# Performance work log

Measured on AMD Instinct MI355X. Metric: run time of the kernel, lower is better.

Reference implementation:

```python
import jax, jax.numpy as jnp
import numpy as np

DIM = 2560
HEADS = 64
HEAD_DIM = 40
TEMB = 512
FF = 4 * DIM
B = 1
S = 1248
TXT = 224
EPS = 1e-6


def _ln(x, eps=EPS):
    # LayerNorm over last dim, no affine (elementwise_affine=False)
    m = jnp.mean(x, axis=-1, keepdims=True)
    v = jnp.mean(jnp.square(x - m), axis=-1, keepdims=True)
    return (x - m) * jax.lax.rsqrt(v + eps)


def setup_inputs() -> dict:
    key = jax.random.key(0)
    ks = jax.random.split(key, 10)
    w = 0.02
    return {
        "hidden_states": jax.random.normal(ks[0], (B, S, DIM), jnp.float32),
        "emb": jax.random.normal(ks[1], (B, TEMB), jnp.float32),
        "attention_mask": jnp.zeros((B, 1, S, S), jnp.float32),
        "adaln_w": jax.random.normal(ks[2], (TEMB, 12 * DIM), jnp.float32) * w,
        "adaln_b": jnp.zeros((12 * DIM,), jnp.float32),
        "qkv_w": jax.random.normal(ks[3], (DIM, 3 * DIM), jnp.float32) * w,
        "qkv_b": jnp.zeros((3 * DIM,), jnp.float32),
        "out_w": jax.random.normal(ks[4], (DIM, DIM), jnp.float32) * w,
        "out_b": jnp.zeros((DIM,), jnp.float32),
        "ff1_w": jax.random.normal(ks[5], (DIM, FF), jnp.float32) * w,
        "ff1_b": jnp.zeros((FF,), jnp.float32),
        "ff2_w": jax.random.normal(ks[6], (FF, DIM), jnp.float32) * w,
        "ff2_b": jnp.zeros((DIM,), jnp.float32),
        "text_length": TXT,
    }


def reference(hidden_states, emb, attention_mask, adaln_w, adaln_b, qkv_w, qkv_b,
              out_w, out_b, ff1_w, ff1_b, ff2_w, ff2_b, text_length):
    b, s, d = hidden_states.shape
    t = text_length

    # adaLN: SiLU -> Linear(time_embed_dim, 12*dim), chunk into 12 [B, dim] pieces
    ada = jax.nn.silu(emb) @ adaln_w + adaln_b
    (sh_msa_i, sc_msa_i, g_msa_i, sh_mlp_i, sc_mlp_i, g_mlp_i,
     sh_msa_t, sc_msa_t, g_msa_t, sh_mlp_t, sc_mlp_t, g_mlp_t) = jnp.split(ada, 12, axis=1)

    def mod(x, shift, scale):
        return x * (1.0 + scale[:, None, :]) + shift[:, None, :]

    # --- attention block ---
    ai = _ln(hidden_states)
    ai = jnp.concatenate([mod(ai[:, :t], sh_msa_t, sc_msa_t),
                          mod(ai[:, t:], sh_msa_i, sc_msa_i)], axis=1)

    qkv = ai @ qkv_w + qkv_b                              # [B, S, 3*D]
    q, k, v = jnp.split(qkv, 3, axis=-1)
    q = q.reshape(b, s, HEADS, HEAD_DIM).transpose(0, 2, 1, 3)  # [B, H, S, hd]
    k = k.reshape(b, s, HEADS, HEAD_DIM).transpose(0, 2, 1, 3)
    v = v.reshape(b, s, HEADS, HEAD_DIM).transpose(0, 2, 1, 3)

    q = _ln(q)  # per-head QK layernorm
    k = _ln(k)

    scores = jnp.einsum("bhqd,bhkd->bhqk", q, k) / (HEAD_DIM ** 0.5)
    scores = scores + attention_mask
    probs = jax.nn.softmax(scores, axis=-1)
    ctx = jnp.einsum("bhqk,bhkd->bhqd", probs, v)
    ctx = ctx.transpose(0, 2, 1, 3).reshape(b, s, d)
    attn_out = ctx @ out_w + out_b

    h = jnp.concatenate([hidden_states[:, :t] + g_msa_t[:, None, :] * attn_out[:, :t],
                         hidden_states[:, t:] + g_msa_i[:, None, :] * attn_out[:, t:]], axis=1)

    # --- MLP block ---
    mi = _ln(h)
    mi = jnp.concatenate([mod(mi[:, :t], sh_mlp_t, sc_mlp_t),
                          mod(mi[:, t:], sh_mlp_i, sc_mlp_i)], axis=1)
    mo = jax.nn.gelu(mi @ ff1_w + ff1_b, approximate=True) @ ff2_w + ff2_b

    h = jnp.concatenate([h[:, :t] + g_mlp_t[:, None, :] * mo[:, :t],
                         h[:, t:] + g_mlp_i[:, None, :] * mo[:, t:]], axis=1)
    return h
```

## Files before the change

### kernel.cpp

```cpp
#include <hip/hip_runtime.h>
#include <cstdint>

typedef float f32x4 __attribute__((ext_vector_type(4)));
typedef __bf16 bf16x8 __attribute__((ext_vector_type(8)));
typedef __bf16 bf16x4 __attribute__((ext_vector_type(4)));

#define S_LEN 1248
#define S_PAD 1280
#define DIMD 2560
#define NHEAD 64
#define HDIM 40
#define T3 7680

__device__ __forceinline__ f32x4 mfma16(bf16x8 a, bf16x8 b, f32x4 c) {
  return __builtin_amdgcn_mfma_f32_16x16x32_bf16(a, b, c, 0, 0, 0);
}

__global__ void k_adaln(const float* __restrict__ emb, const float* __restrict__ W,
                        const float* __restrict__ b, float* __restrict__ ada) {
  __shared__ __attribute__((aligned(16))) float se[512];
  int tid = threadIdx.x;
  for (int i = tid; i < 512; i += 64) {
    float e = emb[i];
    se[i] = e / (1.f + __expf(-e));
  }
  __syncthreads();
  int col = blockIdx.x * 64 + tid;
  float acc = 0.f;
  #pragma unroll 8
  for (int k = 0; k < 512; ++k) acc += se[k] * W[(size_t)k * 30720 + col];
  ada[col] = acc + b[col];
}

__global__ __launch_bounds__(256) void k_trans(const float* __restrict__ W,
                                               __bf16* __restrict__ Wt, int K, int N) {
  __shared__ __attribute__((aligned(16))) float t[64][65];
  int k0 = blockIdx.y * 64, n0 = blockIdx.x * 64;
  int tid = threadIdx.x;
  #pragma unroll
  for (int i = 0; i < 4; ++i) {
    int r = i * 16 + (tid >> 4), c = (tid & 15) * 4;
    const float4 v = *(const float4*)&W[(size_t)(k0 + r) * N + n0 + c];
    t[r][c] = v.x; t[r][c + 1] = v.y; t[r][c + 2] = v.z; t[r][c + 3] = v.w;
  }
  __syncthreads();
  #pragma unroll
  for (int j = 0; j < 4; ++j) {
    int n = j * 16 + (tid >> 4), kk = (tid & 15) * 4;
    bf16x4 o;
    o[0] = (__bf16)t[kk][n];     o[1] = (__bf16)t[kk + 1][n];
    o[2] = (__bf16)t[kk + 2][n]; o[3] = (__bf16)t[kk + 3][n];
    *(bf16x4*)&Wt[(size_t)(n0 + n) * K + k0 + kk] = o;
  }
}

__global__ __launch_bounds__(256) void k_lnmod(const float* __restrict__ X,
                                               const float* __restrict__ ada,
                                               int csh_t, int csc_t, int csh_i, int csc_i,
                                               const int* __restrict__ tlp,
                                               __bf16* __restrict__ Y) {
  int row = blockIdx.x, tid = threadIdx.x;
  const float* x = X + (size_t)row * DIMD;
  float v[10], s = 0.f, s2 = 0.f;
  #pragma unroll
  for (int i = 0; i < 10; ++i) { v[i] = x[tid + i * 256]; s += v[i]; s2 += v[i] * v[i]; }
  #pragma unroll
  for (int m = 1; m < 64; m <<= 1) { s += __shfl_xor(s, m, 64); s2 += __shfl_xor(s2, m, 64); }
  __shared__ float rs[4], rq[4];
  if ((tid & 63) == 0) { rs[tid >> 6] = s; rq[tid >> 6] = s2; }
  __syncthreads();
  s = rs[0] + rs[1] + rs[2] + rs[3];
  s2 = rq[0] + rq[1] + rq[2] + rq[3];
  float mean = s * (1.f / DIMD);
  float rstd = rsqrtf(s2 * (1.f / DIMD) - mean * mean + 1e-6f);
  int txt = *tlp;
  int csh = row < txt ? csh_t : csh_i, csc = row < txt ? csc_t : csc_i;
  #pragma unroll
  for (int i = 0; i < 10; ++i) {
    int col = tid + i * 256;
    float y = (v[i] - mean) * rstd;
    y = y * (1.f + ada[csc * DIMD + col]) + ada[csh * DIMD + col];
    Y[(size_t)row * DIMD + col] = (__bf16)y;
  }
}

template <int EPI>
__global__ __launch_bounds__(256) void k_gemm(
    const __bf16* __restrict__ A, int lda, const __bf16* __restrict__ Bt, int ldb,
    const float* __restrict__ bias, int N, int ksize,
    float* __restrict__ Cf, __bf16* __restrict__ Cb) {
  __shared__ __attribute__((aligned(16))) __bf16 smem[3][2][4096];
  int tid = threadIdx.x;

  unsigned gx = gridDim.x, gy = gridDim.y;
  unsigned nwg = gx * gy * gridDim.z;
  unsigned orig = (blockIdx.z * gy + blockIdx.y) * gx + blockIdx.x;
  unsigned qq = nwg >> 3, r8 = nwg & 7;
  unsigned xcd = orig & 7, loc = orig >> 3;
  unsigned swz = (xcd < r8 ? xcd * (qq + 1) : r8 * (qq + 1) + (xcd - r8) * qq) + loc;
  unsigned bx = swz % gx;
  unsigned rest = swz / gx;
  unsigned by = rest % gy;
  unsigned bz = rest / gy;

  int m0 = bx * 128, n0 = by * 128;
  int kbase = bz * ksize;
  int wave = tid >> 6, lane = tid & 63;
  int wm = (wave & 1) * 64, wn = (wave >> 1) * 64;
  int l15 = lane & 15, l4 = lane >> 4;
  f32x4 acc[4][4] = {};

  auto STG = [&](__bf16* As, __bf16* Bs, int kk) {
    #pragma unroll
    for (int i = 0; i < 2; ++i) {
      int c = tid + i * 256;
      int row = c >> 2, ko = (c & 3) * 8;
      __builtin_amdgcn_global_load_lds(
          (const __attribute__((address_space(1))) unsigned int*)(A + (size_t)(m0 + row) * lda + kk + ko),
          (__attribute__((address_space(3))) unsigned int*)(As + c * 8), 16, 0, 0);
      __builtin_amdgcn_global_load_lds(
          (const __attribute__((address_space(1))) unsigned int*)(Bt + (size_t)(n0 + row) * ldb + kk + ko),
          (__attribute__((address_space(3))) unsigned int*)(Bs + c * 8), 16, 0, 0);
    }
  };

  int nt = ksize >> 5;
  STG(smem[0][0], smem[0][1], kbase);
  STG(smem[1][0], smem[1][1], kbase + 32);
  asm volatile("s_waitcnt vmcnt(4)" ::: "memory");
  __builtin_amdgcn_s_barrier();

  int rb = 0, sb = 2;
  for (int t = 0; t < nt; ++t) {
    if (t + 2 < nt) STG(smem[sb][0], smem[sb][1], kbase + (t + 2) * 32);
    const __bf16* As = smem[rb][0];
    const __bf16* Bs = smem[rb][1];
    bf16x8 af[4], bfr[4];
    #pragma unroll
    for (int s = 0; s < 4; ++s) {
      af[s] = *(const bf16x8*)&As[(wm + s * 16 + l15) * 32 + l4 * 8];
      bfr[s] = *(const bf16x8*)&Bs[(wn + s * 16 + l15) * 32 + l4 * 8];
    }
    __builtin_amdgcn_s_setprio(1);
    #pragma unroll
    for (int i = 0; i < 4; ++i)
      #pragma unroll
      for (int j = 0; j < 4; ++j)
        acc[i][j] = mfma16(af[i], bfr[j], acc[i][j]);
    __builtin_amdgcn_s_setprio(0);
    __builtin_amdgcn_sched_barrier(0);
    if (t + 2 < nt)
      asm volatile("s_waitcnt vmcnt(4)" ::: "memory");
    else
      asm volatile("s_waitcnt vmcnt(0)" ::: "memory");
    __builtin_amdgcn_s_barrier();
    rb = rb == 2 ? 0 : rb + 1;
    sb = sb == 2 ? 0 : sb + 1;
  }

  float* Cfo = Cf;
  if constexpr (EPI == 3) Cfo = Cf + (size_t)bz * S_PAD * N;
  #pragma unroll
  for (int i = 0; i < 4; ++i) {
    #pragma unroll
    for (int r = 0; r < 4; ++r) {
      int rr = m0 + wm + i * 16 + l4 * 4 + r;
      if (rr >= S_LEN) continue;
      #pragma unroll
      for (int j = 0; j < 4; ++j) {
        int col = n0 + wn + j * 16 + l15;
        if constexpr (EPI == 0) {
          Cfo[(size_t)rr * N + col] = acc[i][j][r] + bias[col];
        } else if constexpr (EPI == 3) {
          Cfo[(size_t)rr * N + col] = acc[i][j][r];
        } else {
          float val = acc[i][j][r] + bias[col];
          float u = val + 0.044715f * val * val * val;
          float gl = 0.5f * val * (1.f + tanhf(0.7978845608028654f * u));
          Cb[(size_t)rr * N + col] = (__bf16)gl;
        }
      }
    }
  }
}

__global__ __launch_bounds__(256) void k_red(const float* __restrict__ part,
                                             const float* __restrict__ bias,
                                             const float* __restrict__ resid,
                                             const float* __restrict__ ada,
                                             int g_t, int g_i, const int* __restrict__ tlp,
                                             int N, float* __restrict__ out) {
  int idx = blockIdx.x * 256 + threadIdx.x;
  int perRow = N >> 2;
  int row = idx / perRow;
  int c4 = (idx - row * perRow) << 2;
  if (row >= S_LEN) return;
  int txt = *tlp;
  size_t off = (size_t)row * N + c4;
  const float4 p0 = *(const float4*)&part[off];
  const float4 p1 = *(const float4*)&part[(size_t)S_PAD * N + off];
  const float4 bb = *(const float4*)&bias[c4];
  const float4 rr = *(const float4*)&resid[off];
  const float4 gg = *(const float4*)&ada[(size_t)(row < txt ? g_t : g_i) * DIMD + c4];
  float4 o;
  o.x = rr.x + gg.x * (p0.x + p1.x + bb.x);
  o.y = rr.y + gg.y * (p0.y + p1.y + bb.y);
  o.z = rr.z + gg.z * (p0.z + p1.z + bb.z);
  o.w = rr.w + gg.w * (p0.w + p1.w + bb.w);
  *(float4*)&out[off] = o;
}

__global__ __launch_bounds__(128) void k_qkln(const float* __restrict__ qkv,
                                              __bf16* __restrict__ Qb, __bf16* __restrict__ Kb) {
  __shared__ __attribute__((aligned(16))) float buf[5120];
  int srow = blockIdx.x, tid = threadIdx.x;
  const float* rowp = qkv + (size_t)srow * T3;
  for (int i = tid; i < 1280; i += 128)
    *(float4*)&buf[i * 4] = *(const float4*)&rowp[i * 4];
  __syncthreads();
  int h = tid & 63;
  bool isK = tid >= 64;
  const float* x = buf + (isK ? DIMD : 0) + h * HDIM;
  float xv[40], s = 0.f;
  #pragma unroll
  for (int d = 0; d < 40; ++d) { xv[d] = x[d]; s += xv[d]; }
  float mean = s * (1.f / 40.f);
  float s2 = 0.f;
  #pragma unroll
  for (int d = 0; d < 40; ++d) { float t = xv[d] - mean; s2 += t * t; }
  float rstd = rsqrtf(s2 * (1.f / 40.f) + 1e-6f);
  float scale = isK ? rstd : rstd * 0.15811388300841897f;
  __bf16* dst = (isK ? Kb : Qb) + ((size_t)h * S_PAD + srow) * 64;
  #pragma unroll
  for (int i = 0; i < 5; ++i) {
    bf16x8 w;
    #pragma unroll
    for (int j = 0; j < 8; ++j) w[j] = (__bf16)((xv[i * 8 + j] - mean) * scale);
    *(bf16x8*)&dst[i * 8] = w;
  }
  bf16x8 z = {};
  *(bf16x8*)&dst[40] = z;
  *(bf16x8*)&dst[48] = z;
  *(bf16x8*)&dst[56] = z;
}

__global__ __launch_bounds__(256) void k_vtrans(const float* __restrict__ qkv,
                                                __bf16* __restrict__ Vt) {
  __shared__ __attribute__((aligned(16))) float t[64][41];
  int h = blockIdx.y, s0 = blockIdx.x * 64;
  int tid = threadIdx.x;
  for (int i = tid; i < 64 * 40; i += 256) {
    int sr = i / 40, d = i - sr * 40;
    int srow = s0 + sr;
    t[sr][d] = (srow < S_LEN) ? qkv[(size_t)srow * T3 + 2 * DIMD + h * HDIM + d] : 0.f;
  }
  __syncthreads();
  int d = tid >> 2, sc = (tid & 3) * 16;
  bf16x8 w0 = {}, w1 = {};
  if (d < 40) {
    #pragma unroll
    for (int q = 0; q < 8; ++q) {
      w0[q] = (__bf16)t[sc + q][d];
      w1[q] = (__bf16)t[sc + 8 + q][d];
    }
  } else if (d == 40) {
    #pragma unroll
    for (int q = 0; q < 8; ++q) { w0[q] = (__bf16)1.0f; w1[q] = (__bf16)1.0f; }
  }
  __bf16* dst = Vt + ((size_t)h * 64 + d) * S_PAD + s0 + sc;
  *(bf16x8*)&dst[0] = w0;
  *(bf16x8*)&dst[8] = w1;
}

__global__ __launch_bounds__(256) void k_attn(const __bf16* __restrict__ Qb,
                                              const __bf16* __restrict__ Kb,
                                              const __bf16* __restrict__ Vt,
                                              const float* __restrict__ mask,
                                              __bf16* __restrict__ ctx) {
  __shared__ __attribute__((aligned(16))) __bf16 kvs[2][2][4096];
  __shared__ __attribute__((aligned(16))) __bf16 plds[4][2][1024];
  unsigned orig = blockIdx.y * 10 + blockIdx.x;
  unsigned swz = (orig & 7) * 80 + (orig >> 3);
  int h = swz / 10, q0 = (swz % 10) * 128;
  int tid = threadIdx.x, wave = tid >> 6, lane = tid & 63;
  int l15 = lane & 15, l4 = lane >> 4;
  int qb = q0 + wave * 32;

  const __bf16* Kh = Kb + (size_t)h * S_PAD * 64;
  const __bf16* Vh = Vt + (size_t)h * 64 * S_PAD;

  auto STAGE = [&](int buf, int kv0) {
    #pragma unroll
    for (int i = 0; i < 2; ++i) {
      int c = tid + i * 256;
      int row = c >> 3, col = ((c & 7) ^ (row & 7)) * 8;
      __builtin_amdgcn_global_load_lds(
          (const __attribute__((address_space(1))) unsigned int*)(Kh + (size_t)(kv0 + row) * 64 + col),
          (__attribute__((address_space(3))) unsigned int*)&kvs[buf][0][c * 8], 16, 0, 0);
      __builtin_amdgcn_global_load_lds(
          (const __attribute__((address_space(1))) unsigned int*)(Vh + (size_t)row * S_PAD + kv0 + col),
          (__attribute__((address_space(3))) unsigned int*)&kvs[buf][1][c * 8], 16, 0, 0);
    }
  };

  bf16x8 qf[2][2];
  #pragma unroll
  for (int g = 0; g < 2; ++g) {
    const __bf16* Qp = Qb + ((size_t)h * S_PAD + qb + g * 16 + l15) * 64 + l4 * 8;
    qf[g][0] = *(const bf16x8*)Qp;
    qf[g][1] = *(const bf16x8*)(Qp + 32);
  }
  const float* mrow[2][4];
  #pragma unroll
  for (int g = 0; g < 2; ++g)
    #pragma unroll
    for (int r = 0; r < 4; ++r) {
      int qr = qb + g * 16 + l4 * 4 + r;
      mrow[g][r] = mask + (size_t)(qr < S_LEN ? qr : S_LEN - 1) * S_LEN;
    }
  f32x4 o[2][3] = {};

  STAGE(0, 0);
  for (int t = 0; t < 20; ++t) {
    int kv0 = t * 64;
    if (t < 19) {
      STAGE((t + 1) & 1, kv0 + 64);
      asm volatile("s_waitcnt vmcnt(4)" ::: "memory");
    } else {
      asm volatile("s_waitcnt vmcnt(0)" ::: "memory");
    }
    __builtin_amdgcn_s_barrier();
    const __bf16* Ks = kvs[t & 1][0];
    const __bf16* Vs = kvs[t & 1][1];

    float mreg[2][4][4];
    #pragma unroll
    for (int g = 0; g < 2; ++g)
      #pragma unroll
      for (int ns = 0; ns < 4; ++ns) {
        int kvc = kv0 + ns * 16 + l15;
        int mc = kvc < S_LEN ? kvc : S_LEN - 1;
        #pragma unroll
        for (int r = 0; r < 4; ++r) mreg[g][ns][r] = mrow[g][r][mc];
      }

    bf16x8 kf[4][2];
    #pragma unroll
    for (int ns = 0; ns < 4; ++ns) {
      int kvr = ns * 16 + l15, sw = kvr & 7;
      kf[ns][0] = *(const bf16x8*)((const char*)Ks + kvr * 128 + ((l4 ^ sw) << 4));
      kf[ns][1] = *(const bf16x8*)((const char*)Ks + kvr * 128 + (((4 + l4) ^ sw) << 4));
    }
    bf16x8 vf[3][2];
    #pragma unroll
    for (int d3 = 0; d3 < 3; ++d3) {
      int dr = d3 * 16 + l15, sw = dr & 7;
      vf[d3][0] = *(const bf16x8*)((const char*)Vs + dr * 128 + ((l4 ^ sw) << 4));
      vf[d3][1] = *(const bf16x8*)((const char*)Vs + dr * 128 + (((4 + l4) ^ sw) << 4));
    }

    #pragma unroll
    for (int g = 0; g < 2; ++g) {
      f32x4 sf[4];
      #pragma unroll
      for (int ns = 0; ns < 4; ++ns) {
        f32x4 a = {};
        a = mfma16(qf[g][0], kf[ns][0], a);
        a = mfma16(qf[g][1], kf[ns][1], a);
        sf[ns] = a;
      }
      #pragma unroll
      for (int ns = 0; ns < 4; ++ns) {
        int kvc = kv0 + ns * 16 + l15;
        #pragma unroll
        for (int r = 0; r < 4; ++r) {
          float val = sf[ns][r] - 8.f + mreg[g][ns][r];
          if (kvc >= S_LEN) val = -100.f;
          float e = __expf(val);
          int prow = l4 * 4 + r;
          int boff = (prow * 128 + (ns * 16 + l15) * 2) ^ ((prow & 7) << 4);
          plds[wave][g][boff >> 1] = (__bf16)e;
        }
      }
      int swp = (l15 & 7) << 4;
      int ba = l15 * 128 + l4 * 16;
      bf16x8 pa0 = *(const bf16x8*)((const char*)plds[wave][g] + (ba ^ swp));
      bf16x8 pa1 = *(const bf16x8*)((const char*)plds[wave][g] + ((ba + 64) ^ swp));
      #pragma unroll
      for (int d3 = 0; d3 < 3; ++d3) {
        o[g][d3] = mfma16(pa0, vf[d3][0], o[g][d3]);
        o[g][d3] = mfma16(pa1, vf[d3][1], o[g][d3]);
      }
    }
    __builtin_amdgcn_s_barrier();
  }

  #pragma unroll
  for (int g = 0; g < 2; ++g) {
    #pragma unroll
    for (int r = 0; r < 4; ++r) {
      float sum = __shfl(o[g][2][r], (lane & 0x30) + 8, 64);
      float rinv = 1.f / sum;
      int qr = qb + g * 16 + l4 * 4 + r;
      if (qr < S_LEN) {
        #pragma unroll
        for (int d3 = 0; d3 < 3; ++d3) {
          int d = d3 * 16 + l15;
          if (d < HDIM)
            ctx[(size_t)qr * DIMD + h * HDIM + d] = (__bf16)(o[g][d3][r] * rinv);
        }
      }
    }
  }
}

extern "C" void kernel_launch(void* const* d_in, const int* in_sizes, int n_in,
                              void* d_out, int out_size, void* d_ws, size_t ws_size,
                              hipStream_t stream) {
  const float* hidden  = (const float*)d_in[0];
  const float* emb     = (const float*)d_in[1];
  const float* mask    = (const float*)d_in[2];
  const float* adaln_w = (const float*)d_in[3];
  const float* adaln_b = (const float*)d_in[4];
  const float* qkv_w   = (const float*)d_in[5];
  const float* qkv_b   = (const float*)d_in[6];
  const float* out_w   = (const float*)d_in[7];
  const float* out_b   = (const float*)d_in[8];
  const float* ff1_w   = (const float*)d_in[9];
  const float* ff1_b   = (const float*)d_in[10];
  const float* ff2_w   = (const float*)d_in[11];
  const float* ff2_b   = (const float*)d_in[12];
  const int*   tl      = (const int*)d_in[13];
  (void)in_sizes; (void)n_in; (void)out_size; (void)ws_size;

  char* w = (char*)d_ws;
  size_t off = 0;
  auto alloc = [&](size_t b) { char* p = w + off; off += (b + 255) & ~(size_t)255; return p; };
  float*  ada  = (float*)alloc(30720 * 4);
  __bf16* wT   = (__bf16*)alloc((size_t)10240 * 2560 * 2);
  __bf16* ai   = (__bf16*)alloc((size_t)S_PAD * DIMD * 2);
  float*  qkvf = (float*)alloc((size_t)S_PAD * T3 * 4);
  __bf16* Qb   = (__bf16*)alloc((size_t)NHEAD * S_PAD * 64 * 2);
  __bf16* Kb   = (__bf16*)alloc((size_t)NHEAD * S_PAD * 64 * 2);
  __bf16* Vt   = (__bf16*)alloc((size_t)NHEAD * 64 * S_PAD * 2);
  __bf16* ctxb = (__bf16*)alloc((size_t)S_PAD * DIMD * 2);
  float*  hbuf = (float*)alloc((size_t)S_PAD * DIMD * 4);
  __bf16* mi   = ai;
  __bf16* ff1o = (__bf16*)qkvf;
  float*  part = (float*)Qb;

  k_adaln<<<dim3(480), dim3(64), 0, stream>>>(emb, adaln_w, adaln_b, ada);
  k_lnmod<<<dim3(1248), dim3(256), 0, stream>>>(hidden, ada, 6, 7, 0, 1, tl, ai);
  k_trans<<<dim3(7680 / 64, 2560 / 64), dim3(256), 0, stream>>>(qkv_w, wT, 2560, 7680);
  k_gemm<0><<<dim3(10, 60, 1), dim3(256), 0, stream>>>(ai, 2560, wT, 2560, qkv_b, 7680, 2560,
                                                       qkvf, nullptr);
  k_qkln<<<dim3(1248), dim3(128), 0, stream>>>(qkvf, Qb, Kb);
  k_vtrans<<<dim3(20, 64), dim3(256), 0, stream>>>(qkvf, Vt);
  k_attn<<<dim3(10, 64), dim3(256), 0, stream>>>(Qb, Kb, Vt, mask, ctxb);
  k_trans<<<dim3(2560 / 64, 2560 / 64), dim3(256), 0, stream>>>(out_w, wT, 2560, 2560);
  k_gemm<3><<<dim3(10, 20, 2), dim3(256), 0, stream>>>(ctxb, 2560, wT, 2560, nullptr, 2560, 1280,
                                                       part, nullptr);
  k_red<<<dim3(3120), dim3(256), 0, stream>>>(part, out_b, hidden, ada, 8, 2, tl, 2560, hbuf);
  k_lnmod<<<dim3(1248), dim3(256), 0, stream>>>(hbuf, ada, 9, 10, 3, 4, tl, mi);
  k_trans<<<dim3(10240 / 64, 2560 / 64), dim3(256), 0, stream>>>(ff1_w, wT, 2560, 10240);
  k_gemm<2><<<dim3(10, 80, 1), dim3(256), 0, stream>>>(mi, 2560, wT, 2560, ff1_b, 10240, 2560,
                                                       nullptr, ff1o);
  k_trans<<<dim3(2560 / 64, 10240 / 64), dim3(256), 0, stream>>>(ff2_w, wT, 10240, 2560);
  k_gemm<3><<<dim3(10, 20, 2), dim3(256), 0, stream>>>(ff1o, 10240, wT, 10240, nullptr, 2560, 5120,
                                                       part, nullptr);
  k_red<<<dim3(3120), dim3(256), 0, stream>>>(part, ff2_b, hbuf, ada, 11, 5, tl, 2560, (float*)d_out);
}
```

Baseline: 562.8 us.

## Use 8-wave 256-row GEMM tiles with swizzled LDS and split-phase pipeline

Replaces the 128x128, 4-wave GEMM with a 512-thread kernel using 256xBN tiles (BN=256 for QKV and FF1, 128 for the split-K projections). A/B tiles are staged into a 4-slot LDS ring with an XOR swizzle on the k offset to avoid bank conflicts. Each k-step is split into two half-MFMA phases, with the A and B prefetches interleaved between them. The goal is more operand reuse per load and fewer LDS conflicts, at the cost of fewer workgroups on the M=1248 problem (more padding waste), extra barriers, and higher register pressure.

```diff
diff --git a/kernel.cpp b/kernel.cpp
--- a/kernel.cpp
+++ b/kernel.cpp
@@ -84,12 +84,15 @@
   }
 }
 
-template <int EPI>
-__global__ __launch_bounds__(256) void k_gemm(
+template <int BN, int EPI>
+__global__ __launch_bounds__(512, 2) void k_gemm8(
     const __bf16* __restrict__ A, int lda, const __bf16* __restrict__ Bt, int ldb,
     const float* __restrict__ bias, int N, int ksize,
     float* __restrict__ Cf, __bf16* __restrict__ Cb) {
-  __shared__ __attribute__((aligned(16))) __bf16 smem[3][2][4096];
+  constexpr int MF = (BN == 256) ? 8 : 4;
+  constexpr int BLOADS = BN / 128;
+  __shared__ __attribute__((aligned(16))) __bf16 ldsA[4][8192];
+  __shared__ __attribute__((aligned(16))) __bf16 ldsB[4][BN * 32];
   int tid = threadIdx.x;
 
   unsigned gx = gridDim.x, gy = gridDim.y;
@@ -103,78 +106,118 @@
   unsigned by = rest % gy;
   unsigned bz = rest / gy;
 
-  int m0 = bx * 128, n0 = by * 128;
-  int kbase = bz * ksize;
-  int wave = tid >> 6, lane = tid & 63;
-  int wm = (wave & 1) * 64, wn = (wave >> 1) * 64;
-  int l15 = lane & 15, l4 = lane >> 4;
-  f32x4 acc[4][4] = {};
-
-  auto STG = [&](__bf16* As, __bf16* Bs, int kk) {
+  int m0 = bx * 256, n0 = by * BN;
+  const __bf16* Ab = A + (size_t)bz * ksize;
+  const __bf16* Bb = Bt + (size_t)bz * ksize;
+  int wid = tid >> 6, lane = tid & 63, l15 = lane & 15, l4 = lane >> 4;
+  int wrow = (BN == 256) ? (wid >> 2) * 128 : (wid >> 1) * 64;
+  int wcol = (BN == 256) ? (wid & 3) * 64 : (wid & 1) * 64;
+
+  f32x4 acc[MF][4] = {};
+
+  int grow = tid >> 2;
+  int gcb = (tid & 3) * 16;
+  auto STAGE_A = [&](int slot, int kk) {
     #pragma unroll
     for (int i = 0; i < 2; ++i) {
-      int c = tid + i * 256;
-      int row = c >> 2, ko = (c & 3) * 8;
+      int row = i * 128 + grow;
+      int se = kk + ((gcb ^ (((row >> 3) & 1) << 5)) >> 1);
       __builtin_amdgcn_global_load_lds(
-          (const __attribute__((address_space(1))) unsigned int*)(A + (size_t)(m0 + row) * lda + kk + ko),
-          (__attribute__((address_space(3))) unsigned int*)(As + c * 8), 16, 0, 0);
+          (const __attribute__((address_space(1))) unsigned int*)(Ab + (size_t)(m0 + row) * lda + se),
+          (__attribute__((address_space(3))) unsigned int*)((char*)ldsA[slot] + i * 8192 + tid * 16),
+          16, 0, 0);
+    }
+  };
+  auto STAGE_B = [&](int slot, int kk) {
+    #pragma unroll
+    for (int i = 0; i < BLOADS; ++i) {
+      int row = i * 128 + grow;
+      int se = kk + ((gcb ^ (((row >> 3) & 1) << 5)) >> 1);
       __builtin_amdgcn_global_load_lds(
-          (const __attribute__((address_space(1))) unsigned int*)(Bt + (size_t)(n0 + row) * ldb + kk + ko),
-          (__attribute__((address_space(3))) unsigned int*)(Bs + c * 8), 16, 0, 0);
+          (const __attribute__((address_space(1))) unsigned int*)(Bb + (size_t)(n0 + row) * ldb + se),
+          (__attribute__((address_space(3))) unsigned int*)((char*)ldsB[slot] + i * 8192 + tid * 16),
+          16, 0, 0);
     }
   };
 
-  int nt = ksize >> 5;
-  STG(smem[0][0], smem[0][1], kbase);
-  STG(smem[1][0], smem[1][1], kbase + 32);
-  asm volatile("s_waitcnt vmcnt(4)" ::: "memory");
+  int nslots = ksize >> 5;
+  STAGE_A(0, 0); STAGE_B(0, 0);
+  STAGE_A(1, 32); STAGE_B(1, 32);
+  if constexpr (BN == 256) asm volatile("s_waitcnt vmcnt(4)" ::: "memory");
+  else                     asm volatile("s_waitcnt vmcnt(3)" ::: "memory");
   __builtin_amdgcn_s_barrier();
 
-  int rb = 0, sb = 2;
-  for (int t = 0; t < nt; ++t) {
-    if (t + 2 < nt) STG(smem[sb][0], smem[sb][1], kbase + (t + 2) * 32);
-    const __bf16* As = smem[rb][0];
-    const __bf16* Bs = smem[rb][1];
-    bf16x8 af[4], bfr[4];
-    #pragma unroll
-    for (int s = 0; s < 4; ++s) {
-      af[s] = *(const bf16x8*)&As[(wm + s * 16 + l15) * 32 + l4 * 8];
-      bfr[s] = *(const bf16x8*)&Bs[(wn + s * 16 + l15) * 32 + l4 * 8];
-    }
+  int asw = ((l15 >> 3) & 1) << 5;
+  int cbb = l4 * 16;
+
+  for (int s = 0; s < nslots; ++s) {
+    int sl = s & 3;
+    int kst = (s + 2) * 32;
+    bool st = kst < ksize;
+    int slw = (s + 2) & 3;
+
+    bf16x8 bfr[4], af[MF / 2];
+    #pragma unroll
+    for (int nf = 0; nf < 4; ++nf) {
+      int row = wcol + nf * 16 + l15;
+      bfr[nf] = *(const bf16x8*)((const char*)ldsB[sl] + row * 64 + (cbb ^ asw));
+    }
+    #pragma unroll
+    for (int mf = 0; mf < MF / 2; ++mf) {
+      int row = wrow + mf * 16 + l15;
+      af[mf] = *(const bf16x8*)((const char*)ldsA[sl] + row * 64 + (cbb ^ asw));
+    }
+    if (st) STAGE_A(slw, kst);
+    __builtin_amdgcn_s_barrier();
     __builtin_amdgcn_s_setprio(1);
     #pragma unroll
-    for (int i = 0; i < 4; ++i)
-      #pragma unroll
-      for (int j = 0; j < 4; ++j)
-        acc[i][j] = mfma16(af[i], bfr[j], acc[i][j]);
+    for (int mf = 0; mf < MF / 2; ++mf)
+      #pragma unroll
+      for (int nf = 0; nf < 4; ++nf)
+        acc[mf][nf] = mfma16(af[mf], bfr[nf], acc[mf][nf]);
     __builtin_amdgcn_s_setprio(0);
-    __builtin_amdgcn_sched_barrier(0);
-    if (t + 2 < nt)
-      asm volatile("s_waitcnt vmcnt(4)" ::: "memory");
-    else
+    __builtin_amdgcn_s_barrier();
+
+    #pragma unroll
+    for (int mf = 0; mf < MF / 2; ++mf) {
+      int row = wrow + (MF / 2 + mf) * 16 + l15;
+      af[mf] = *(const bf16x8*)((const char*)ldsA[sl] + row * 64 + (cbb ^ asw));
+    }
+    if (st) STAGE_B(slw, kst);
+    __builtin_amdgcn_s_barrier();
+    __builtin_amdgcn_s_setprio(1);
+    #pragma unroll
+    for (int mf = 0; mf < MF / 2; ++mf)
+      #pragma unroll
+      for (int nf = 0; nf < 4; ++nf)
+        acc[MF / 2 + mf][nf] = mfma16(af[mf], bfr[nf], acc[MF / 2 + mf][nf]);
+    __builtin_amdgcn_s_setprio(0);
+    if (st) {
+      if constexpr (BN == 256) asm volatile("s_waitcnt vmcnt(4)" ::: "memory");
+      else                     asm volatile("s_waitcnt vmcnt(3)" ::: "memory");
+    } else {
       asm volatile("s_waitcnt vmcnt(0)" ::: "memory");
+    }
     __builtin_amdgcn_s_barrier();
-    rb = rb == 2 ? 0 : rb + 1;
-    sb = sb == 2 ? 0 : sb + 1;
   }
 
   float* Cfo = Cf;
   if constexpr (EPI == 3) Cfo = Cf + (size_t)bz * S_PAD * N;
   #pragma unroll
-  for (int i = 0; i < 4; ++i) {
+  for (int mf = 0; mf < MF; ++mf) {
     #pragma unroll
     for (int r = 0; r < 4; ++r) {
-      int rr = m0 + wm + i * 16 + l4 * 4 + r;
+      int rr = m0 + wrow + mf * 16 + l4 * 4 + r;
       if (rr >= S_LEN) continue;
       #pragma unroll
-      for (int j = 0; j < 4; ++j) {
-        int col = n0 + wn + j * 16 + l15;
+      for (int nf = 0; nf < 4; ++nf) {
+        int col = n0 + wcol + nf * 16 + l15;
         if constexpr (EPI == 0) {
-          Cfo[(size_t)rr * N + col] = acc[i][j][r] + bias[col];
+          Cfo[(size_t)rr * N + col] = acc[mf][nf][r] + bias[col];
         } else if constexpr (EPI == 3) {
-          Cfo[(size_t)rr * N + col] = acc[i][j][r];
+          Cfo[(size_t)rr * N + col] = acc[mf][nf][r];
         } else {
-          float val = acc[i][j][r] + bias[col];
+          float val = acc[mf][nf][r] + bias[col];
           float u = val + 0.044715f * val * val * val;
           float gl = 0.5f * val * (1.f + tanhf(0.7978845608028654f * u));
           Cb[(size_t)rr * N + col] = (__bf16)gl;
@@ -452,21 +495,21 @@
   k_adaln<<<dim3(480), dim3(64), 0, stream>>>(emb, adaln_w, adaln_b, ada);
   k_lnmod<<<dim3(1248), dim3(256), 0, stream>>>(hidden, ada, 6, 7, 0, 1, tl, ai);
   k_trans<<<dim3(7680 / 64, 2560 / 64), dim3(256), 0, stream>>>(qkv_w, wT, 2560, 7680);
-  k_gemm<0><<<dim3(10, 60, 1), dim3(256), 0, stream>>>(ai, 2560, wT, 2560, qkv_b, 7680, 2560,
-                                                       qkvf, nullptr);
+  k_gemm8<256, 0><<<dim3(5, 30, 1), dim3(512), 0, stream>>>(ai, 2560, wT, 2560, qkv_b, 7680, 2560,
+                                                            qkvf, nullptr);
   k_qkln<<<dim3(1248), dim3(128), 0, stream>>>(qkvf, Qb, Kb);
   k_vtrans<<<dim3(20, 64), dim3(256), 0, stream>>>(qkvf, Vt);
   k_attn<<<dim3(10, 64), dim3(256), 0, stream>>>(Qb, Kb, Vt, mask, ctxb);
   k_trans<<<dim3(2560 / 64, 2560 / 64), dim3(256), 0, stream>>>(out_w, wT, 2560, 2560);
-  k_gemm<3><<<dim3(10, 20, 2), dim3(256), 0, stream>>>(ctxb, 2560, wT, 2560, nullptr, 2560, 1280,
-                                                       part, nullptr);
+  k_gemm8<128, 3><<<dim3(5, 20, 2), dim3(512), 0, stream>>>(ctxb, 2560, wT, 2560, nullptr, 2560, 1280,
+                                                            part, nullptr);
   k_red<<<dim3(3120), dim3(256), 0, stream>>>(part, out_b, hidden, ada, 8, 2, tl, 2560, hbuf);
   k_lnmod<<<dim3(1248), dim3(256), 0, stream>>>(hbuf, ada, 9, 10, 3, 4, tl, mi);
   k_trans<<<dim3(10240 / 64, 2560 / 64), dim3(256), 0, stream>>>(ff1_w, wT, 2560, 10240);
-  k_gemm<2><<<dim3(10, 80, 1), dim3(256), 0, stream>>>(mi, 2560, wT, 2560, ff1_b, 10240, 2560,
-                                                       nullptr, ff1o);
+  k_gemm8<256, 2><<<dim3(5, 40, 1), dim3(512), 0, stream>>>(mi, 2560, wT, 2560, ff1_b, 10240, 2560,
+                                                            nullptr, ff1o);
   k_trans<<<dim3(2560 / 64, 10240 / 64), dim3(256), 0, stream>>>(ff2_w, wT, 10240, 2560);
-  k_gemm<3><<<dim3(10, 20, 2), dim3(256), 0, stream>>>(ff1o, 10240, wT, 10240, nullptr, 2560, 5120,
-                                                       part, nullptr);
+  k_gemm8<128, 3><<<dim3(5, 20, 2), dim3(512), 0, stream>>>(ff1o, 10240, wT, 10240, nullptr, 2560, 5120,
+                                                            part, nullptr);
   k_red<<<dim3(3120), dim3(256), 0, stream>>>(part, ff2_b, hbuf, ada, 11, 5, tl, 2560, (float*)d_out);
 }
```

Result: slower. 625.7 us (+11.2%).

## Add 160x256-tile 512-thread GEMM for QKV and FF1 projections

Applied to the files above, without the earlier changes.

Adds a new GEMM kernel with 160x256 output tiles, 8 waves per block, a triple-buffered LDS pipeline fed by direct global-to-LDS loads, XOR-swizzled LDS rows and XCD-aware block remapping. The QKV and FF1 projections now use it, giving grids of 8x30 and 8x40 blocks instead of 10x60 and 10x80. Eight row tiles of 160 cover exactly 1280 padded rows, and the larger tile reuses more data per load. The cost is higher register pressure from 20 accumulator fragments per wave and fewer blocks in flight, which may limit latency hiding.

```diff
diff --git a/kernel.cpp b/kernel.cpp
--- a/kernel.cpp
+++ b/kernel.cpp
@@ -81,6 +81,120 @@
     float y = (v[i] - mean) * rstd;
     y = y * (1.f + ada[csc * DIMD + col]) + ada[csh * DIMD + col];
     Y[(size_t)row * DIMD + col] = (__bf16)y;
+  }
+}
+
+template <int EPI>
+__global__ __launch_bounds__(512, 2) void k_gemm9(
+    const __bf16* __restrict__ A, int lda, const __bf16* __restrict__ Bt, int ldb,
+    const float* __restrict__ bias, int N, int K,
+    float* __restrict__ Cf, __bf16* __restrict__ Cb) {
+  __shared__ __attribute__((aligned(16))) __bf16 ldsA[3][160 * 32];
+  __shared__ __attribute__((aligned(16))) __bf16 ldsB[3][256 * 32];
+  int tid = threadIdx.x;
+
+  unsigned gx = gridDim.x, gy = gridDim.y;
+  unsigned nwg = gx * gy;
+  unsigned orig = blockIdx.y * gx + blockIdx.x;
+  unsigned qq = nwg >> 3, r8 = nwg & 7;
+  unsigned xcd = orig & 7, loc = orig >> 3;
+  unsigned swz = (xcd < r8 ? xcd * (qq + 1) : r8 * (qq + 1) + (xcd - r8) * qq) + loc;
+  unsigned bx = swz % gx, by = swz / gx;
+
+  int m0 = bx * 160, n0 = by * 256;
+  int wid = tid >> 6, lane = tid & 63, l15 = lane & 15, l4 = lane >> 4;
+  int wm = (wid >> 2) * 80, wn = (wid & 3) * 64;
+
+  f32x4 acc[5][4] = {};
+
+  auto STAGE = [&](int slot, int kk) {
+    {
+      int a = tid, row = a >> 2;
+      int cb = ((a & 3) << 4) ^ ((row & 3) << 4);
+      __builtin_amdgcn_global_load_lds(
+          (const __attribute__((address_space(1))) unsigned int*)(A + (size_t)(m0 + row) * lda + kk + (cb >> 1)),
+          (__attribute__((address_space(3))) unsigned int*)((char*)ldsA[slot] + a * 16), 16, 0, 0);
+      if (tid < 128) {
+        int a2 = 512 + tid, row2 = a2 >> 2;
+        int cb2 = ((a2 & 3) << 4) ^ ((row2 & 3) << 4);
+        __builtin_amdgcn_global_load_lds(
+            (const __attribute__((address_space(1))) unsigned int*)(A + (size_t)(m0 + row2) * lda + kk + (cb2 >> 1)),
+            (__attribute__((address_space(3))) unsigned int*)((char*)ldsA[slot] + a2 * 16), 16, 0, 0);
+      }
+    }
+    #pragma unroll
+    for (int i = 0; i < 2; ++i) {
+      int b = tid + i * 512, row = b >> 2;
+      int cb = ((b & 3) << 4) ^ ((row & 3) << 4);
+      __builtin_amdgcn_global_load_lds(
+          (const __attribute__((address_space(1))) unsigned int*)(Bt + (size_t)(n0 + row) * ldb + kk + (cb >> 1)),
+          (__attribute__((address_space(3))) unsigned int*)((char*)ldsB[slot] + b * 16), 16, 0, 0);
+    }
+  };
+
+  int nslots = K >> 5;
+  STAGE(0, 0);
+  STAGE(1, 32);
+  if (wid < 2) asm volatile("s_waitcnt vmcnt(4)" ::: "memory");
+  else         asm volatile("s_waitcnt vmcnt(3)" ::: "memory");
+  __builtin_amdgcn_s_barrier();
+
+  int sl = 0;
+  for (int t = 0; t < nslots; ++t) {
+    int kst = (t + 2) * 32;
+    bool st = kst < K;
+    if (st) {
+      int slw = sl + 2; if (slw >= 3) slw -= 3;
+      STAGE(slw, kst);
+    }
+    bf16x8 af[5], bfr[4];
+    #pragma unroll
+    for (int mf = 0; mf < 5; ++mf) {
+      int row = wm + mf * 16 + l15;
+      af[mf] = *(const bf16x8*)((const char*)ldsA[sl] + row * 64 + ((l4 * 16) ^ ((row & 3) << 4)));
+    }
+    #pragma unroll
+    for (int nf = 0; nf < 4; ++nf) {
+      int row = wn + nf * 16 + l15;
+      bfr[nf] = *(const bf16x8*)((const char*)ldsB[sl] + row * 64 + ((l4 * 16) ^ ((row & 3) << 4)));
+    }
+    __builtin_amdgcn_s_setprio(1);
+    #pragma unroll
+    for (int mf = 0; mf < 5; ++mf)
+      #pragma unroll
+      for (int nf = 0; nf < 4; ++nf)
+        acc[mf][nf] = mfma16(af[mf], bfr[nf], acc[mf][nf]);
+    __builtin_amdgcn_s_setprio(0);
+    __builtin_amdgcn_sched_barrier(0);
+    if (st) {
+      if (wid < 2) asm volatile("s_waitcnt vmcnt(4)" ::: "memory");
+      else         asm volatile("s_waitcnt vmcnt(3)" ::: "memory");
+    } else {
+      asm volatile("s_waitcnt vmcnt(0)" ::: "memory");
+    }
+    __builtin_amdgcn_s_barrier();
+    ++sl; if (sl >= 3) sl = 0;
+  }
+
+  #pragma unroll
+  for (int mf = 0; mf < 5; ++mf) {
+    #pragma unroll
+    for (int r = 0; r < 4; ++r) {
+      int rr = m0 + wm + mf * 16 + l4 * 4 + r;
+      if (rr >= S_LEN) continue;
+      #pragma unroll
+      for (int nf = 0; nf < 4; ++nf) {
+        int col = n0 + wn + nf * 16 + l15;
+        float val = acc[mf][nf][r] + bias[col];
+        if constexpr (EPI == 0) {
+          Cf[(size_t)rr * N + col] = val;
+        } else {
+          float u = val + 0.044715f * val * val * val;
+          float gl = 0.5f * val * (1.f + tanhf(0.7978845608028654f * u));
+          Cb[(size_t)rr * N + col] = (__bf16)gl;
+        }
+      }
+    }
   }
 }
 
@@ -452,8 +566,8 @@
   k_adaln<<<dim3(480), dim3(64), 0, stream>>>(emb, adaln_w, adaln_b, ada);
   k_lnmod<<<dim3(1248), dim3(256), 0, stream>>>(hidden, ada, 6, 7, 0, 1, tl, ai);
   k_trans<<<dim3(7680 / 64, 2560 / 64), dim3(256), 0, stream>>>(qkv_w, wT, 2560, 7680);
-  k_gemm<0><<<dim3(10, 60, 1), dim3(256), 0, stream>>>(ai, 2560, wT, 2560, qkv_b, 7680, 2560,
-                                                       qkvf, nullptr);
+  k_gemm9<0><<<dim3(8, 30), dim3(512), 0, stream>>>(ai, 2560, wT, 2560, qkv_b, 7680, 2560,
+                                                    qkvf, nullptr);
   k_qkln<<<dim3(1248), dim3(128), 0, stream>>>(qkvf, Qb, Kb);
   k_vtrans<<<dim3(20, 64), dim3(256), 0, stream>>>(qkvf, Vt);
   k_attn<<<dim3(10, 64), dim3(256), 0, stream>>>(Qb, Kb, Vt, mask, ctxb);
@@ -463,8 +577,8 @@
   k_red<<<dim3(3120), dim3(256), 0, stream>>>(part, out_b, hidden, ada, 8, 2, tl, 2560, hbuf);
   k_lnmod<<<dim3(1248), dim3(256), 0, stream>>>(hbuf, ada, 9, 10, 3, 4, tl, mi);
   k_trans<<<dim3(10240 / 64, 2560 / 64), dim3(256), 0, stream>>>(ff1_w, wT, 2560, 10240);
-  k_gemm<2><<<dim3(10, 80, 1), dim3(256), 0, stream>>>(mi, 2560, wT, 2560, ff1_b, 10240, 2560,
-                                                       nullptr, ff1o);
+  k_gemm9<2><<<dim3(8, 40), dim3(512), 0, stream>>>(mi, 2560, wT, 2560, ff1_b, 10240, 2560,
+                                                    nullptr, ff1o);
   k_trans<<<dim3(2560 / 64, 10240 / 64), dim3(256), 0, stream>>>(ff2_w, wT, 10240, 2560);
   k_gemm<3><<<dim3(10, 20, 2), dim3(256), 0, stream>>>(ff1o, 10240, wT, 10240, nullptr, 2560, 5120,
                                                        part, nullptr);
```

After: 633.5 us. 12.6% more time.
